# Kernel tuning notes

Hardware: AMD Instinct MI355X
Metric: run time of the kernel (lower is better)

Reference implementation:

```python
import jax, jax.numpy as jnp
import numpy as np

CE_TEMP = 1.0
SIMW_TEMP = 0.1
NSEG = 2048
EPS = 1e-8
NEG = jnp.float32(-1e30)


def setup_inputs() -> dict:
    key = jax.random.key(0)
    k1, k2, k3, k4, k5, k6 = jax.random.split(key, 6)
    N, C, H, W, Ch, S = 2, 19, 128, 128, 256, NSEG
    inputs_plbl = jax.random.normal(k1, (N, C, H, W), dtype=jnp.float32)
    feats_plbl = jax.random.normal(k2, (N, Ch, H, W), dtype=jnp.float32)
    inputs = jax.random.normal(k3, (N, C, H, W), dtype=jnp.float32)
    # multi-hot targets per superpixel; ~2.3 active classes on average -> many multi-hot rows
    targets = jax.random.bernoulli(k4, 0.12, (N, S, C)).astype(jnp.float32)
    superpixels = jax.random.randint(k5, (N, H, W), 0, S, dtype=jnp.int32)
    spmasks = jax.random.bernoulli(k6, 0.5, (N, H, W))
    return {"inputs_plbl": inputs_plbl, "feats_plbl": feats_plbl, "inputs": inputs,
            "targets": targets, "superpixels": superpixels, "spmasks": spmasks}


def _per_image(out_plbl, feat, out, trg_table, sp, mask):
    # out_plbl: [HW,C] softmax'd pseudo-label probs; feat: [HW,Ch]; out: [HW,C];
    # trg_table: [S,C] multi-hot; sp: [HW] int superpixel ids; mask: [HW] bool
    HW, C = out_plbl.shape
    S = trg_table.shape[0]
    trg_pix = trg_table[sp]                                  # [HW,C]
    multi_spx = trg_table.sum(-1) > 1.0                      # [S]
    valid = mask & multi_spx[sp]                             # == spmask & multi-hot mask

    # scatter_max: argmax pixel per (superpixel, class) among valid pixels
    scores = jnp.where(valid[:, None], out_plbl, NEG)
    seg_max = jax.ops.segment_max(scores, sp, num_segments=S)       # [S,C]
    is_max = valid[:, None] & (scores >= seg_max[sp])
    cand = jnp.where(is_max, jnp.arange(HW, dtype=jnp.int32)[:, None], HW)
    proto_idx = jax.ops.segment_min(cand, sp, num_segments=S)       # [S,C]
    proto_idx = jnp.clip(proto_idx, 0, HW - 1)

    # prototype features and per-pixel similarities to own-superpixel class prototypes
    proto_feat = feat[proto_idx]                             # [S,C,Ch]
    pf_pix = proto_feat[sp]                                  # [HW,C,Ch] (dominant intermediate)
    sim = jnp.einsum('kcd,kd->kc', pf_pix, feat) / SIMW_TEMP  # [HW,C]

    # scatter_softmax over the active classes of the pixel's superpixel
    active = trg_pix > 0.0
    w_multi = jax.nn.softmax(jnp.where(active, sim, NEG), axis=-1)
    w_row = jnp.where(active, w_multi, trg_pix)              # inactive entries keep 0
    w = jnp.where(valid[:, None], w_row, trg_pix)            # non-multi pixels keep one-hot
    w = jax.lax.stop_gradient(w)                             # original computes weights under no_grad

    ce = -jnp.log(out + EPS)                                 # [HW,C]
    contrib = jnp.where(mask[:, None], w * ce, 0.0)
    any_valid = jnp.any(valid)                               # image skipped if no multi-hot masked pixel
    loss_i = jnp.where(any_valid, contrib.sum(), 0.0)
    cnt_i = jnp.where(any_valid, mask.sum(), 0)
    return loss_i, cnt_i


def reference(inputs_plbl, feats_plbl, inputs, targets, superpixels, spmasks):
    N, C, H, W = inputs_plbl.shape
    Ch = feats_plbl.shape[1]
    out_plbl = jax.nn.softmax(inputs_plbl / CE_TEMP, axis=1).transpose(0, 2, 3, 1).reshape(N, -1, C)
    feats = feats_plbl.transpose(0, 2, 3, 1).reshape(N, -1, Ch)
    out = jax.nn.softmax(inputs / CE_TEMP, axis=1).transpose(0, 2, 3, 1).reshape(N, -1, C)
    sp = superpixels.reshape(N, -1)
    mask = spmasks.reshape(N, -1)
    loss_i, cnt_i = jax.vmap(_per_image)(out_plbl, feats, out, targets, sp, mask)
    total = loss_i.sum()
    cnt = cnt_i.sum()
    return jnp.where(cnt > 0, total / jnp.maximum(cnt, 1).astype(jnp.float32), 0.0)
```

## Files before the change

kernel.cpp:

```cpp
#include <hip/hip_runtime.h>
#include <cstdint>
#include <cstddef>

#define NN   2
#define CC   19
#define HWD  16384
#define CH   256
#define SS   2048
#define BCAP 32

#define MAIN_BLKS  (2 * NN * HWD / 256)
#define TRAN_BLKS  ((HWD / 64) * (CH / 64) * NN)

__device__ __forceinline__ unsigned short f2bf(float x) {
    unsigned u = __float_as_uint(x);
    return (unsigned short)((u + 0x7FFFu + ((u >> 16) & 1u)) >> 16);
}
__device__ __forceinline__ float bf2f(unsigned short h) {
    return __uint_as_float(((unsigned)h) << 16);
}

__global__ __launch_bounds__(256) void k_fused(
        const float* __restrict__ xp, const float* __restrict__ xi,
        const float* __restrict__ F, const float* __restrict__ trg,
        const int* __restrict__ sp, const int* __restrict__ msk,
        int* __restrict__ sp_cnt, unsigned short* __restrict__ bucket,
        float* __restrict__ plbl_pm, float* __restrict__ ce_pm,
        unsigned short* __restrict__ feat_t, int* __restrict__ cnt,
        int* __restrict__ vcnt, float* __restrict__ slots) {
    __shared__ float tile[64][65];
    __shared__ unsigned char vld[64];

    if (blockIdx.x < MAIN_BLKS) {
        int gid = blockIdx.x * blockDim.x + threadIdx.x;
        int partB = (gid >= NN * HWD);
        int idx = partB ? gid - NN * HWD : gid;
        int n = idx >> 14;
        int k = idx & (HWD - 1);
        int lane = threadIdx.x & 63;
        int m = (msk[idx] != 0);
        int s = sp[idx];
        const float* t = trg + ((size_t)n * SS + s) * CC;
        int mu = 0;
        if (m) {
            float ts = 0.f;
            #pragma unroll
            for (int c = 0; c < CC; ++c) ts += t[c];
            mu = (ts > 1.0f);
        }
        int valid = m && mu;

        if (!partB) {
            unsigned long long mb = __ballot(m);
            unsigned long long vb = __ballot(valid);
            if (valid) {
                int cell = n * SS + s;
                int pos = atomicAdd(&sp_cnt[cell], 1);
                if (pos < BCAP) bucket[(size_t)cell * BCAP + pos] = (unsigned short)k;
                const float* a = xp + (size_t)n * CC * HWD + k;
                float v[CC];
                float mx = -1e30f;
                #pragma unroll
                for (int c = 0; c < CC; ++c) { v[c] = a[(size_t)c * HWD]; mx = fmaxf(mx, v[c]); }
                float su = 0.f;
                #pragma unroll
                for (int c = 0; c < CC; ++c) { v[c] = expf(v[c] - mx); su += v[c]; }
                float inv = 1.f / su;
                float* op = plbl_pm + (size_t)idx * CC;
                #pragma unroll
                for (int c = 0; c < CC; ++c) op[c] = v[c] * inv;
            }
            if (lane == 0) {
                if (mb) atomicAdd(&cnt[n], __popcll(mb));
                if (vb) atomicAdd(&vcnt[n], __popcll(vb));
            }
        } else {
            float contrib = 0.f;
            if (m) {
                const float* b = xi + (size_t)n * CC * HWD + k;
                float v[CC];
                float mx = -1e30f;
                #pragma unroll
                for (int c = 0; c < CC; ++c) { v[c] = b[(size_t)c * HWD]; mx = fmaxf(mx, v[c]); }
                float su = 0.f;
                #pragma unroll
                for (int c = 0; c < CC; ++c) su += expf(v[c] - mx);
                float lsu = logf(su);
                if (mu) {
                    float* cp = ce_pm + (size_t)idx * CC;
                    #pragma unroll
                    for (int c = 0; c < CC; ++c) cp[c] = lsu - (v[c] - mx);
                } else {
                    #pragma unroll
                    for (int c = 0; c < CC; ++c) contrib += t[c] * (lsu - (v[c] - mx));
                }
            }
            #pragma unroll
            for (int off = 32; off >= 1; off >>= 1) contrib += __shfl_xor(contrib, off);
            if (lane == 0 && contrib != 0.f)
                atomicAdd(&slots[n * 128 + ((idx >> 6) & 127)], contrib);
        }
    } else {
        int b2 = blockIdx.x - MAIN_BLKS;
        int k0 = (b2 & 255) * 64;
        int d0 = ((b2 >> 8) & 3) * 64;
        int n  = b2 >> 10;
        int tx = threadIdx.x & 63, ty = threadIdx.x >> 6;
        const float* src = F + (size_t)n * CH * HWD;
        unsigned short* dst = feat_t + (size_t)n * HWD * CH;

        if (ty == 0) {
            int pix = n * HWD + k0 + tx;
            int m = (msk[pix] != 0);
            int flag = 0;
            if (m) {
                int s = sp[pix];
                const float* t = trg + ((size_t)n * SS + s) * CC;
                float ts = 0.f;
                #pragma unroll
                for (int c = 0; c < CC; ++c) ts += t[c];
                flag = (ts > 1.0f);
            }
            vld[tx] = (unsigned char)flag;
        }
        #pragma unroll
        for (int i = 0; i < 16; ++i) {
            int dd = ty + 4 * i;
            tile[dd][tx] = src[(size_t)(d0 + dd) * HWD + (k0 + tx)];
        }
        __syncthreads();
        #pragma unroll
        for (int i = 0; i < 16; ++i) {
            int kk = ty + 4 * i;
            if (vld[kk]) dst[(size_t)(k0 + kk) * CH + (d0 + tx)] = f2bf(tile[tx][kk]);
        }
    }
}

__global__ __launch_bounds__(256) void k_sim(
        const unsigned short* __restrict__ feat_t, const float* __restrict__ ce_pm,
        const float* __restrict__ plbl_pm, const float* __restrict__ trg,
        const int* __restrict__ sp_cnt, const unsigned short* __restrict__ bucket,
        float* __restrict__ slots) {
    int id = blockIdx.x;
    int cnt_c = sp_cnt[id];
    if (cnt_c == 0) return;
    cnt_c = min(cnt_c, BCAP);
    int n    = id >> 11;
    int tid  = threadIdx.x;
    int lane = tid & 63;
    int wv   = tid >> 6;

    __shared__ float protoF[CC][CH];
    __shared__ float s_bv[4][CC];
    __shared__ int   s_bi[4][CC];
    __shared__ int   s_proto[CC];
    __shared__ int   actc[CC];

    float t = (lane < CC) ? trg[(size_t)id * CC + lane] : 0.f;
    unsigned long long act = __ballot(t > 0.f);
    int nact = __popcll(act);
    int apos = __popcll(act & ((1ull << lane) - 1ull));
    if ((act >> lane) & 1ull) actc[apos] = lane;
    int mypix = (lane < cnt_c) ? (int)bucket[(size_t)id * BCAP + lane] : 0;

    float bv = -1e30f;
    int   bi = HWD;
    for (int i = wv; i < cnt_c; i += 4) {
        int pix = __shfl(mypix, i);
        if (lane < CC) {
            float v = plbl_pm[((size_t)(n * HWD + pix)) * CC + lane];
            if (v > bv || (v == bv && pix < bi)) { bv = v; bi = pix; }
        }
    }
    if (lane < CC) { s_bv[wv][lane] = bv; s_bi[wv][lane] = bi; }
    __syncthreads();
    if (lane < CC) {
        bv = -1e30f; bi = HWD;
        #pragma unroll
        for (int j = 0; j < 4; ++j) {
            float v = s_bv[j][lane];
            int   p = s_bi[j][lane];
            if (v > bv || (v == bv && p < bi)) { bv = v; bi = p; }
        }
        if ((act >> lane) & 1ull) s_proto[apos] = bi;
    }
    __syncthreads();

    for (int a = wv; a < nact; a += 4) {
        int p = s_proto[a];
        ushort4 q = ((const ushort4*)(feat_t + ((size_t)(n * HWD + p)) * CH))[lane];
        float4 v = make_float4(bf2f(q.x), bf2f(q.y), bf2f(q.z), bf2f(q.w));
        ((float4*)(&protoF[a][0]))[lane] = v;
    }
    __syncthreads();

    float wcontrib = 0.f;
    for (int i = wv; i < cnt_c; i += 4) {
        int pix = __shfl(mypix, i);
        float ce = (lane < nact)
                 ? ce_pm[((size_t)(n * HWD + pix)) * CC + actc[lane]] : 0.f;
        ushort4 q = ((const ushort4*)(feat_t + ((size_t)(n * HWD + pix)) * CH))[lane];
        float4 f = make_float4(bf2f(q.x), bf2f(q.y), bf2f(q.z), bf2f(q.w));
        float mysim = -1e30f;
        for (int a = 0; a < nact; ++a) {
            float4 pf = ((const float4*)(&protoF[a][0]))[lane];
            float d = f.x * pf.x + f.y * pf.y + f.z * pf.z + f.w * pf.w;
            #pragma unroll
            for (int off = 32; off >= 1; off >>= 1) d += __shfl_xor(d, off);
            if (lane == a) mysim = d * 10.0f;
        }
        float mx = mysim;
        #pragma unroll
        for (int off = 32; off >= 1; off >>= 1) mx = fmaxf(mx, __shfl_xor(mx, off));
        float e = (lane < nact) ? expf(mysim - mx) : 0.f;
        float se = e;
        #pragma unroll
        for (int off = 32; off >= 1; off >>= 1) se += __shfl_xor(se, off);
        float c1 = (e / se) * ce;
        #pragma unroll
        for (int off = 32; off >= 1; off >>= 1) c1 += __shfl_xor(c1, off);
        wcontrib += c1;
    }
    if (lane == 0 && wcontrib != 0.f)
        atomicAdd(&slots[n * 128 + (id & 127)], wcontrib);
}

__global__ void k_final(const float* __restrict__ slots, const int* __restrict__ cnt,
                        const int* __restrict__ vcnt, float* __restrict__ out) {
    __shared__ float red[2];
    int t = threadIdx.x;
    int w = t >> 6;
    int lane = t & 63;
    float v = slots[w * 128 + lane] + slots[w * 128 + lane + 64];
    #pragma unroll
    for (int off = 32; off >= 1; off >>= 1) v += __shfl_xor(v, off);
    if (lane == 0) red[w] = v;
    __syncthreads();
    if (t == 0) {
        float total = 0.f;
        int c = 0;
        for (int n = 0; n < NN; ++n)
            if (vcnt[n] > 0) { total += red[n]; c += cnt[n]; }
        out[0] = (c > 0) ? total / (float)c : 0.f;
    }
}

extern "C" void kernel_launch(void* const* d_in, const int* in_sizes, int n_in,
                              void* d_out, int out_size, void* d_ws, size_t ws_size,
                              hipStream_t stream) {
    const float* inputs_plbl = (const float*)d_in[0];
    const float* feats_plbl  = (const float*)d_in[1];
    const float* inputs      = (const float*)d_in[2];
    const float* targets     = (const float*)d_in[3];
    const int*   superpixels = (const int*)d_in[4];
    const int*   spmasks     = (const int*)d_in[5];
    float* out = (float*)d_out;

    char* ws = (char*)d_ws;
    int*   sp_cnt = (int*)ws;
    int*   cnt    = (int*)(ws + 16384);
    int*   vcnt   = (int*)(ws + 16392);
    float* slots  = (float*)(ws + 16416);
    unsigned short* bucket = (unsigned short*)(ws + 17440);
    float* plbl_pm = (float*)(ws + 279584);
    float* ce_pm   = (float*)(ws + 2769952);
    unsigned short* feat_t = (unsigned short*)(ws + 5260320);

    hipMemsetAsync(ws, 0, 17440, stream);

    k_fused<<<MAIN_BLKS + TRAN_BLKS, 256, 0, stream>>>(
        inputs_plbl, inputs, feats_plbl, targets, superpixels, spmasks,
        sp_cnt, bucket, plbl_pm, ce_pm, feat_t, cnt, vcnt, slots);
    k_sim<<<NN * SS, 256, 0, stream>>>(feat_t, ce_pm, plbl_pm, targets,
                                       sp_cnt, bucket, slots);
    k_final<<<1, 128, 0, stream>>>(slots, cnt, vcnt, out);
}
```

Before: 129.5 us.

## Fuse prototype argmax into atomics, precompute active masks, one wave per superpixel

Adds an init kernel that zeroes the workspace and precomputes a per-superpixel active-class bitmask with a multi-hot flag. This replaces the repeated 19-float target reads in the fused and transpose paths. The per-(superpixel,class) argmax prototype is now computed in the fused kernel with 64-bit packed atomicMax (value high, inverted index low), so the plbl_pm buffer and the block-level reduction in k_sim are gone. k_sim is restructured to one wavefront per superpixel, with four prototypes held in registers, software prefetch of the next pixel, and no shared memory or block syncs. The trade-off is 19 global 64-bit atomics per valid pixel and a larger zero-initialised region.

```diff
diff --git a/kernel.cpp b/kernel.cpp
--- a/kernel.cpp
+++ b/kernel.cpp
@@ -12,6 +12,16 @@
 #define MAIN_BLKS  (2 * NN * HWD / 256)
 #define TRAN_BLKS  ((HWD / 64) * (CH / 64) * NN)
 
+#define OFF_SPCNT  622592
+#define OFF_CNT    638976
+#define OFF_VCNT   638984
+#define OFF_SLOTS  638992
+#define ZERO_F4    40001
+#define OFF_ACT    640016
+#define OFF_BUCKET 656400
+#define OFF_CE     918544
+#define OFF_FEAT   3408912
+
 __device__ __forceinline__ unsigned short f2bf(float x) {
     unsigned u = __float_as_uint(x);
     return (unsigned short)((u + 0x7FFFu + ((u >> 16) & 1u)) >> 16);
@@ -20,14 +30,33 @@
     return __uint_as_float(((unsigned)h) << 16);
 }
 
+__global__ __launch_bounds__(256) void k_init(const float* __restrict__ trg,
+                                              unsigned* __restrict__ actmask,
+                                              float4* __restrict__ zb) {
+    int tid = blockIdx.x * 256 + threadIdx.x;
+    float4 z = make_float4(0.f, 0.f, 0.f, 0.f);
+    for (int i = tid; i < ZERO_F4; i += 64 * 256) zb[i] = z;
+    if (tid < NN * SS) {
+        const float* t = trg + (size_t)tid * CC;
+        unsigned mk = 0;
+        int na = 0;
+        #pragma unroll
+        for (int c = 0; c < CC; ++c) {
+            if (t[c] > 0.f) { mk |= (1u << c); ++na; }
+        }
+        if (na > 1) mk |= 0x80000000u;
+        actmask[tid] = mk;
+    }
+}
+
 __global__ __launch_bounds__(256) void k_fused(
         const float* __restrict__ xp, const float* __restrict__ xi,
-        const float* __restrict__ F, const float* __restrict__ trg,
+        const float* __restrict__ F, const unsigned* __restrict__ actmask,
         const int* __restrict__ sp, const int* __restrict__ msk,
         int* __restrict__ sp_cnt, unsigned short* __restrict__ bucket,
-        float* __restrict__ plbl_pm, float* __restrict__ ce_pm,
-        unsigned short* __restrict__ feat_t, int* __restrict__ cnt,
-        int* __restrict__ vcnt, float* __restrict__ slots) {
+        unsigned long long* __restrict__ amax,
+        float* __restrict__ ce_pm, unsigned short* __restrict__ feat_t,
+        int* __restrict__ cnt, int* __restrict__ vcnt, float* __restrict__ slots) {
     __shared__ float tile[64][65];
     __shared__ unsigned char vld[64];
 
@@ -40,21 +69,15 @@
         int lane = threadIdx.x & 63;
         int m = (msk[idx] != 0);
         int s = sp[idx];
-        const float* t = trg + ((size_t)n * SS + s) * CC;
-        int mu = 0;
-        if (m) {
-            float ts = 0.f;
-            #pragma unroll
-            for (int c = 0; c < CC; ++c) ts += t[c];
-            mu = (ts > 1.0f);
-        }
+        unsigned flag = m ? actmask[(n << 11) + s] : 0u;
+        int mu = (int)(flag >> 31);
         int valid = m && mu;
 
         if (!partB) {
             unsigned long long mb = __ballot(m);
             unsigned long long vb = __ballot(valid);
             if (valid) {
-                int cell = n * SS + s;
+                int cell = (n << 11) + s;
                 int pos = atomicAdd(&sp_cnt[cell], 1);
                 if (pos < BCAP) bucket[(size_t)cell * BCAP + pos] = (unsigned short)k;
                 const float* a = xp + (size_t)n * CC * HWD + k;
@@ -66,9 +89,14 @@
                 #pragma unroll
                 for (int c = 0; c < CC; ++c) { v[c] = expf(v[c] - mx); su += v[c]; }
                 float inv = 1.f / su;
-                float* op = plbl_pm + (size_t)idx * CC;
-                #pragma unroll
-                for (int c = 0; c < CC; ++c) op[c] = v[c] * inv;
+                unsigned long long low = (unsigned long long)(unsigned)(HWD - k);
+                unsigned long long* arow = amax + (size_t)cell * CC;
+                #pragma unroll
+                for (int c = 0; c < CC; ++c) {
+                    unsigned long long key =
+                        ((unsigned long long)__float_as_uint(v[c] * inv) << 32) | low;
+                    atomicMax(&arow[c], key);
+                }
             }
             if (lane == 0) {
                 if (mb) atomicAdd(&cnt[n], __popcll(mb));
@@ -92,7 +120,8 @@
                     for (int c = 0; c < CC; ++c) cp[c] = lsu - (v[c] - mx);
                 } else {
                     #pragma unroll
-                    for (int c = 0; c < CC; ++c) contrib += t[c] * (lsu - (v[c] - mx));
+                    for (int c = 0; c < CC; ++c)
+                        if ((flag >> c) & 1u) contrib += lsu - (v[c] - mx);
                 }
             }
             #pragma unroll
@@ -112,16 +141,9 @@
         if (ty == 0) {
             int pix = n * HWD + k0 + tx;
             int m = (msk[pix] != 0);
-            int flag = 0;
-            if (m) {
-                int s = sp[pix];
-                const float* t = trg + ((size_t)n * SS + s) * CC;
-                float ts = 0.f;
-                #pragma unroll
-                for (int c = 0; c < CC; ++c) ts += t[c];
-                flag = (ts > 1.0f);
-            }
-            vld[tx] = (unsigned char)flag;
+            int fl = 0;
+            if (m) fl = (int)(actmask[(n << 11) + sp[pix]] >> 31);
+            vld[tx] = (unsigned char)fl;
         }
         #pragma unroll
         for (int i = 0; i < 16; ++i) {
@@ -139,91 +161,134 @@
 
 __global__ __launch_bounds__(256) void k_sim(
         const unsigned short* __restrict__ feat_t, const float* __restrict__ ce_pm,
-        const float* __restrict__ plbl_pm, const float* __restrict__ trg,
+        const unsigned long long* __restrict__ amax, const unsigned* __restrict__ actmask,
         const int* __restrict__ sp_cnt, const unsigned short* __restrict__ bucket,
         float* __restrict__ slots) {
-    int id = blockIdx.x;
+    int lane = threadIdx.x & 63;
+    int id = (blockIdx.x << 2) + (threadIdx.x >> 6);
     int cnt_c = sp_cnt[id];
     if (cnt_c == 0) return;
     cnt_c = min(cnt_c, BCAP);
-    int n    = id >> 11;
-    int tid  = threadIdx.x;
-    int lane = tid & 63;
-    int wv   = tid >> 6;
-
-    __shared__ float protoF[CC][CH];
-    __shared__ float s_bv[4][CC];
-    __shared__ int   s_bi[4][CC];
-    __shared__ int   s_proto[CC];
-    __shared__ int   actc[CC];
-
-    float t = (lane < CC) ? trg[(size_t)id * CC + lane] : 0.f;
-    unsigned long long act = __ballot(t > 0.f);
-    int nact = __popcll(act);
-    int apos = __popcll(act & ((1ull << lane) - 1ull));
-    if ((act >> lane) & 1ull) actc[apos] = lane;
+    int n = id >> 11;
+    unsigned act = actmask[id] & 0x7FFFFu;
+    int nact = __popc(act);
+
+    int myc = 0;
+    {
+        int seen = 0;
+        #pragma unroll
+        for (int c = 0; c < CC; ++c) {
+            int b = (int)((act >> c) & 1u);
+            if (b && seen == lane) myc = c;
+            seen += b;
+        }
+    }
+    int ppix = 0;
+    if (lane < nact) {
+        unsigned long long key = amax[(size_t)id * CC + myc];
+        ppix = HWD - (int)(unsigned)(key & 0xFFFFFFFFull);
+    }
+    const unsigned short* Fb = feat_t + (size_t)n * HWD * CH;
     int mypix = (lane < cnt_c) ? (int)bucket[(size_t)id * BCAP + lane] : 0;
-
-    float bv = -1e30f;
-    int   bi = HWD;
-    for (int i = wv; i < cnt_c; i += 4) {
-        int pix = __shfl(mypix, i);
-        if (lane < CC) {
-            float v = plbl_pm[((size_t)(n * HWD + pix)) * CC + lane];
-            if (v > bv || (v == bv && pix < bi)) { bv = v; bi = pix; }
-        }
-    }
-    if (lane < CC) { s_bv[wv][lane] = bv; s_bi[wv][lane] = bi; }
-    __syncthreads();
-    if (lane < CC) {
-        bv = -1e30f; bi = HWD;
-        #pragma unroll
-        for (int j = 0; j < 4; ++j) {
-            float v = s_bv[j][lane];
-            int   p = s_bi[j][lane];
-            if (v > bv || (v == bv && p < bi)) { bv = v; bi = p; }
-        }
-        if ((act >> lane) & 1ull) s_proto[apos] = bi;
-    }
-    __syncthreads();
-
-    for (int a = wv; a < nact; a += 4) {
-        int p = s_proto[a];
-        ushort4 q = ((const ushort4*)(feat_t + ((size_t)(n * HWD + p)) * CH))[lane];
-        float4 v = make_float4(bf2f(q.x), bf2f(q.y), bf2f(q.z), bf2f(q.w));
-        ((float4*)(&protoF[a][0]))[lane] = v;
-    }
-    __syncthreads();
-
     float wcontrib = 0.f;
-    for (int i = wv; i < cnt_c; i += 4) {
-        int pix = __shfl(mypix, i);
-        float ce = (lane < nact)
-                 ? ce_pm[((size_t)(n * HWD + pix)) * CC + actc[lane]] : 0.f;
-        ushort4 q = ((const ushort4*)(feat_t + ((size_t)(n * HWD + pix)) * CH))[lane];
-        float4 f = make_float4(bf2f(q.x), bf2f(q.y), bf2f(q.z), bf2f(q.w));
-        float mysim = -1e30f;
-        for (int a = 0; a < nact; ++a) {
-            float4 pf = ((const float4*)(&protoF[a][0]))[lane];
-            float d = f.x * pf.x + f.y * pf.y + f.z * pf.z + f.w * pf.w;
-            #pragma unroll
-            for (int off = 32; off >= 1; off >>= 1) d += __shfl_xor(d, off);
-            if (lane == a) mysim = d * 10.0f;
-        }
-        float mx = mysim;
-        #pragma unroll
-        for (int off = 32; off >= 1; off >>= 1) mx = fmaxf(mx, __shfl_xor(mx, off));
-        float e = (lane < nact) ? expf(mysim - mx) : 0.f;
-        float se = e;
-        #pragma unroll
-        for (int off = 32; off >= 1; off >>= 1) se += __shfl_xor(se, off);
-        float c1 = (e / se) * ce;
-        #pragma unroll
-        for (int off = 32; off >= 1; off >>= 1) c1 += __shfl_xor(c1, off);
-        wcontrib += c1;
+
+    if (nact <= 4) {
+        int p0 = __shfl(ppix, 0), p1 = __shfl(ppix, 1);
+        int p2 = __shfl(ppix, 2), p3 = __shfl(ppix, 3);
+        ushort4 q0 = ((const ushort4*)(Fb + (size_t)p0 * CH))[lane];
+        ushort4 q1 = ((const ushort4*)(Fb + (size_t)p1 * CH))[lane];
+        ushort4 q2 = ((const ushort4*)(Fb + (size_t)p2 * CH))[lane];
+        ushort4 q3 = ((const ushort4*)(Fb + (size_t)p3 * CH))[lane];
+        float4 pf0 = make_float4(bf2f(q0.x), bf2f(q0.y), bf2f(q0.z), bf2f(q0.w));
+        float4 pf1 = make_float4(bf2f(q1.x), bf2f(q1.y), bf2f(q1.z), bf2f(q1.w));
+        float4 pf2 = make_float4(bf2f(q2.x), bf2f(q2.y), bf2f(q2.z), bf2f(q2.w));
+        float4 pf3 = make_float4(bf2f(q3.x), bf2f(q3.y), bf2f(q3.z), bf2f(q3.w));
+
+        int pix = __shfl(mypix, 0);
+        ushort4 q = ((const ushort4*)(Fb + (size_t)pix * CH))[lane];
+        float cen = (lane < nact) ? ce_pm[((size_t)(n * HWD + pix)) * CC + myc] : 0.f;
+        for (int i = 0; i < cnt_c; ++i) {
+            float4 f = make_float4(bf2f(q.x), bf2f(q.y), bf2f(q.z), bf2f(q.w));
+            float ce = cen;
+            if (i + 1 < cnt_c) {
+                int pixn = __shfl(mypix, i + 1);
+                q = ((const ushort4*)(Fb + (size_t)pixn * CH))[lane];
+                cen = (lane < nact) ? ce_pm[((size_t)(n * HWD + pixn)) * CC + myc] : 0.f;
+            }
+            float d0 = f.x * pf0.x + f.y * pf0.y + f.z * pf0.z + f.w * pf0.w;
+            float d1 = f.x * pf1.x + f.y * pf1.y + f.z * pf1.z + f.w * pf1.w;
+            float d2 = f.x * pf2.x + f.y * pf2.y + f.z * pf2.z + f.w * pf2.w;
+            float d3 = f.x * pf3.x + f.y * pf3.y + f.z * pf3.z + f.w * pf3.w;
+            #pragma unroll
+            for (int off = 32; off >= 1; off >>= 1) {
+                d0 += __shfl_xor(d0, off);
+                d1 += __shfl_xor(d1, off);
+                d2 += __shfl_xor(d2, off);
+                d3 += __shfl_xor(d3, off);
+            }
+            float dsel = (lane == 0) ? d0 : (lane == 1) ? d1 : (lane == 2) ? d2 : d3;
+            float mysim = (lane < nact) ? dsel * 10.0f : -1e30f;
+            float mx = fmaxf(mysim, __shfl_xor(mysim, 1));
+            mx = fmaxf(mx, __shfl_xor(mx, 2));
+            float e = (lane < nact) ? expf(mysim - mx) : 0.f;
+            float se = e;
+            se += __shfl_xor(se, 1);
+            se += __shfl_xor(se, 2);
+            float c1 = (e / se) * ce;
+            c1 += __shfl_xor(c1, 1);
+            c1 += __shfl_xor(c1, 2);
+            wcontrib += c1;
+        }
+    } else {
+        for (int i = 0; i < cnt_c; ++i) {
+            int pix = __shfl(mypix, i);
+            float ce = (lane < nact) ? ce_pm[((size_t)(n * HWD + pix)) * CC + myc] : 0.f;
+            ushort4 q = ((const ushort4*)(Fb + (size_t)pix * CH))[lane];
+            float4 f = make_float4(bf2f(q.x), bf2f(q.y), bf2f(q.z), bf2f(q.w));
+            float mysim = -1e30f;
+            for (int a0 = 0; a0 < nact; a0 += 4) {
+                int p0 = __shfl(ppix, a0);
+                int p1 = __shfl(ppix, a0 + 1);
+                int p2 = __shfl(ppix, a0 + 2);
+                int p3 = __shfl(ppix, a0 + 3);
+                ushort4 q0 = ((const ushort4*)(Fb + (size_t)p0 * CH))[lane];
+                ushort4 q1 = ((const ushort4*)(Fb + (size_t)p1 * CH))[lane];
+                ushort4 q2 = ((const ushort4*)(Fb + (size_t)p2 * CH))[lane];
+                ushort4 q3 = ((const ushort4*)(Fb + (size_t)p3 * CH))[lane];
+                float4 pf0 = make_float4(bf2f(q0.x), bf2f(q0.y), bf2f(q0.z), bf2f(q0.w));
+                float4 pf1 = make_float4(bf2f(q1.x), bf2f(q1.y), bf2f(q1.z), bf2f(q1.w));
+                float4 pf2 = make_float4(bf2f(q2.x), bf2f(q2.y), bf2f(q2.z), bf2f(q2.w));
+                float4 pf3 = make_float4(bf2f(q3.x), bf2f(q3.y), bf2f(q3.z), bf2f(q3.w));
+                float d0 = f.x * pf0.x + f.y * pf0.y + f.z * pf0.z + f.w * pf0.w;
+                float d1 = f.x * pf1.x + f.y * pf1.y + f.z * pf1.z + f.w * pf1.w;
+                float d2 = f.x * pf2.x + f.y * pf2.y + f.z * pf2.z + f.w * pf2.w;
+                float d3 = f.x * pf3.x + f.y * pf3.y + f.z * pf3.z + f.w * pf3.w;
+                #pragma unroll
+                for (int off = 32; off >= 1; off >>= 1) {
+                    d0 += __shfl_xor(d0, off);
+                    d1 += __shfl_xor(d1, off);
+                    d2 += __shfl_xor(d2, off);
+                    d3 += __shfl_xor(d3, off);
+                }
+                float dsel = (lane == a0) ? d0 : (lane == a0 + 1) ? d1
+                           : (lane == a0 + 2) ? d2 : d3;
+                if (lane >= a0 && lane < a0 + 4 && lane < nact) mysim = dsel * 10.0f;
+            }
+            float mx = mysim;
+            #pragma unroll
+            for (int off = 16; off >= 1; off >>= 1) mx = fmaxf(mx, __shfl_xor(mx, off));
+            float e = (lane < nact) ? expf(mysim - mx) : 0.f;
+            float se = e;
+            #pragma unroll
+            for (int off = 16; off >= 1; off >>= 1) se += __shfl_xor(se, off);
+            float c1 = (e / se) * ce;
+            #pragma unroll
+            for (int off = 16; off >= 1; off >>= 1) c1 += __shfl_xor(c1, off);
+            wcontrib += c1;
+        }
     }
     if (lane == 0 && wcontrib != 0.f)
-        atomicAdd(&slots[n * 128 + (id & 127)], wcontrib);
+        atomicAdd(&slots[(n << 7) + (id & 127)], wcontrib);
 }
 
 __global__ void k_final(const float* __restrict__ slots, const int* __restrict__ cnt,
@@ -258,21 +323,21 @@
     float* out = (float*)d_out;
 
     char* ws = (char*)d_ws;
-    int*   sp_cnt = (int*)ws;
-    int*   cnt    = (int*)(ws + 16384);
-    int*   vcnt   = (int*)(ws + 16392);
-    float* slots  = (float*)(ws + 16416);
-    unsigned short* bucket = (unsigned short*)(ws + 17440);
-    float* plbl_pm = (float*)(ws + 279584);
-    float* ce_pm   = (float*)(ws + 2769952);
-    unsigned short* feat_t = (unsigned short*)(ws + 5260320);
-
-    hipMemsetAsync(ws, 0, 17440, stream);
-
+    unsigned long long* amax = (unsigned long long*)ws;
+    int*   sp_cnt  = (int*)(ws + OFF_SPCNT);
+    int*   cnt     = (int*)(ws + OFF_CNT);
+    int*   vcnt    = (int*)(ws + OFF_VCNT);
+    float* slots   = (float*)(ws + OFF_SLOTS);
+    unsigned* actmask = (unsigned*)(ws + OFF_ACT);
+    unsigned short* bucket = (unsigned short*)(ws + OFF_BUCKET);
+    float* ce_pm   = (float*)(ws + OFF_CE);
+    unsigned short* feat_t = (unsigned short*)(ws + OFF_FEAT);
+
+    k_init<<<64, 256, 0, stream>>>(targets, actmask, (float4*)ws);
     k_fused<<<MAIN_BLKS + TRAN_BLKS, 256, 0, stream>>>(
-        inputs_plbl, inputs, feats_plbl, targets, superpixels, spmasks,
-        sp_cnt, bucket, plbl_pm, ce_pm, feat_t, cnt, vcnt, slots);
-    k_sim<<<NN * SS, 256, 0, stream>>>(feat_t, ce_pm, plbl_pm, targets,
-                                       sp_cnt, bucket, slots);
+        inputs_plbl, inputs, feats_plbl, actmask, superpixels, spmasks,
+        sp_cnt, bucket, amax, ce_pm, feat_t, cnt, vcnt, slots);
+    k_sim<<<NN * SS / 4, 256, 0, stream>>>(feat_t, ce_pm, amax, actmask,
+                                           sp_cnt, bucket, slots);
     k_final<<<1, 128, 0, stream>>>(slots, cnt, vcnt, out);
 }
```

Result: no change. 130.0 us (+0.4%).
